# Kernel tuning notes

Measured on AMD Instinct MI355X. Metric: run time of the kernel, lower is better.

The kernel has to match this reference:

```python
import jax, jax.numpy as jnp
import numpy as np

NUM_HEADS = 8
HEAD_DIM = 64      # key_dim = tts_embed_dims // num_heads
TOKEN_NUM = 10
EMBED_DIMS = 512   # tts_embed_dims (num_units)
QUERY_DIM = 256    # tts_embed_dims // 2
BATCH = 131072


def setup_inputs() -> dict:
    key = jax.random.key(0)
    k1, k2, k3, k4 = jax.random.split(key, 4)
    inputs = jax.random.normal(k1, (BATCH, QUERY_DIM), dtype=jnp.float32)
    # nn.Parameter init.normal_(mean=0, std=0.5)
    embed = 0.5 * jax.random.normal(k2, (TOKEN_NUM, HEAD_DIM), dtype=jnp.float32)
    # nn.Linear weights are [out_features, in_features]
    Wq = jax.random.normal(k3, (EMBED_DIMS, QUERY_DIM), dtype=jnp.float32) * (QUERY_DIM ** -0.5)
    Wk = jax.random.normal(k4, (EMBED_DIMS, HEAD_DIM), dtype=jnp.float32) * (HEAD_DIM ** -0.5)
    return {"inputs": inputs, "embed": embed, "Wq": Wq, "Wk": Wk}


def reference(inputs, embed, Wq, Wk):
    # Faithful to this fork: values = raw tanh(embed) keys (W_value unused),
    # and NO softmax on the attention scores.
    N = inputs.shape[0]
    h, d, T = NUM_HEADS, HEAD_DIM, TOKEN_NUM
    keys_raw = jnp.tanh(embed)                       # [T, d] (shared across batch)

    q = inputs @ Wq.T                                # [N, E]
    q = q.reshape(N, h, d)                           # split heads (T_q == 1 squeezed)

    k = keys_raw @ Wk.T                              # [T, E]
    k = k.reshape(T, h, d)                           # [T, h, d]

    scale = HEAD_DIM ** 0.5                          # self.key_dim ** 0.5
    # scores: [h, N, 1, T] -> store as [h, N, T]
    scores = jnp.einsum('nhd,thd->hnt', q, k) / scale

    # out per head: scores @ values, values = keys_raw [T, d]
    out = jnp.einsum('hnt,td->nhd', scores, keys_raw)  # [N, h, d]
    style_embed = out.reshape(N, 1, h * d)             # concat heads -> [N, 1, E]
    attn_score = scores[:, :, None, :]                 # [h, N, 1, T]
    return style_embed, attn_score
```

## Files before the change

kernel.cpp:

```cpp
#include <hip/hip_runtime.h>
#include <math.h>

#define N_QDIM 256
#define N_EDIM 512
#define N_HEADS 8
#define N_HDIM 64
#define N_TOK 10
#define NJ 80

__global__ __launch_bounds__(256) void precompute_kernel(
    const float* __restrict__ embed, const float* __restrict__ Wq,
    const float* __restrict__ Wk, float* __restrict__ Ws,
    float* __restrict__ keysOut)
{
    __shared__ float skeys[N_TOK * N_HDIM];
    __shared__ float sK[N_TOK * N_EDIM];
    const int tid = threadIdx.x;

    for (int i = tid; i < N_TOK * N_HDIM; i += 256) {
        float v = tanhf(embed[i]);
        skeys[i] = v;
        if (blockIdx.x == 0) keysOut[i] = v;
    }
    __syncthreads();

    for (int i = tid; i < N_TOK * N_EDIM; i += 256) {
        int t = i >> 9;
        int e = i & 511;
        float s = 0.f;
        #pragma unroll
        for (int d = 0; d < N_HDIM; d++)
            s += skeys[t * N_HDIM + d] * Wk[e * N_HDIM + d];
        sK[i] = s;
    }
    __syncthreads();

    int v = blockIdx.x * 256 + tid;
    int qd = v / NJ;
    int j  = v - qd * NJ;
    int h  = j / N_TOK;
    int t  = j - h * N_TOK;
    float s = 0.f;
    #pragma unroll
    for (int d = 0; d < N_HDIM; d++)
        s += Wq[(h * N_HDIM + d) * N_QDIM + qd] * sK[t * N_EDIM + h * N_HDIM + d];
    Ws[qd * NJ + j] = s * 0.125f;
}

__global__ __launch_bounds__(256) void main_kernel(
    const float* __restrict__ inputs, const float* __restrict__ Ws,
    const float* __restrict__ keys, float* __restrict__ outStyle,
    float* __restrict__ outAttn, int N)
{
    __shared__ float smem[128 * 81];
    float* sA = smem;
    float* sB = smem + 32 * 132;

    const int tid = threadIdx.x;
    const int tc = tid & 15;
    const int tr = tid >> 4;
    const int n0 = blockIdx.x * 128;
    const float* A = inputs + (size_t)n0 * N_QDIM;

    float acc[8][5];
    #pragma unroll
    for (int i = 0; i < 8; i++)
        #pragma unroll
        for (int j = 0; j < 5; j++) acc[i][j] = 0.f;

    for (int kb = 0; kb < N_QDIM; kb += 32) {
        __syncthreads();
        #pragma unroll
        for (int it = 0; it < 4; it++) {
            int flat = it * 256 + tid;
            int row = flat >> 3;
            int ch  = flat & 7;
            float4 v = *(const float4*)(A + row * N_QDIM + kb + ch * 4);
            int k = ch * 4;
            sA[(k + 0) * 132 + row] = v.x;
            sA[(k + 1) * 132 + row] = v.y;
            sA[(k + 2) * 132 + row] = v.z;
            sA[(k + 3) * 132 + row] = v.w;
        }
        #pragma unroll
        for (int it = 0; it < 3; it++) {
            int f = it * 256 + tid;
            if (f < 640)
                *(float4*)(sB + f * 4) = *(const float4*)(Ws + kb * NJ + f * 4);
        }
        __syncthreads();
        #pragma unroll
        for (int k = 0; k < 32; k++) {
            float4 a0 = *(const float4*)(sA + k * 132 + tr * 8);
            float4 a1 = *(const float4*)(sA + k * 132 + tr * 8 + 4);
            float b[5];
            #pragma unroll
            for (int j = 0; j < 5; j++) b[j] = sB[k * NJ + tc * 5 + j];
            float a[8] = {a0.x, a0.y, a0.z, a0.w, a1.x, a1.y, a1.z, a1.w};
            #pragma unroll
            for (int i = 0; i < 8; i++)
                #pragma unroll
                for (int j = 0; j < 5; j++)
                    acc[i][j] += a[i] * b[j];
        }
    }

    __syncthreads();
    float* sS = smem;
    #pragma unroll
    for (int i = 0; i < 8; i++) {
        int row = tr * 8 + i;
        #pragma unroll
        for (int j = 0; j < 5; j++)
            sS[row * 81 + tc * 5 + j] = acc[i][j];
    }
    __syncthreads();

    #pragma unroll
    for (int h = 0; h < N_HEADS; h++) {
        float* dst = outAttn + (size_t)h * N * N_TOK + (size_t)n0 * N_TOK;
        for (int i = tid; i < 128 * N_TOK; i += 256) {
            int row = i / N_TOK;
            int t = i - row * N_TOK;
            dst[i] = sS[row * 81 + h * N_TOK + t];
        }
    }

    float4 kr[N_TOK];
    #pragma unroll
    for (int t = 0; t < N_TOK; t++)
        kr[t] = *(const float4*)(keys + t * N_HDIM + tc * 4);

    for (int i = 0; i < 8; i++) {
        int row = tr * 8 + i;
        #pragma unroll
        for (int h = 0; h < N_HEADS; h++) {
            float4 o = {0.f, 0.f, 0.f, 0.f};
            #pragma unroll
            for (int t = 0; t < N_TOK; t++) {
                float s = sS[row * 81 + h * N_TOK + t];
                o.x += s * kr[t].x;
                o.y += s * kr[t].y;
                o.z += s * kr[t].z;
                o.w += s * kr[t].w;
            }
            *(float4*)(outStyle + (size_t)(n0 + row) * N_EDIM + h * N_HDIM + tc * 4) = o;
        }
    }
}

extern "C" void kernel_launch(void* const* d_in, const int* in_sizes, int n_in,
                              void* d_out, int out_size, void* d_ws, size_t ws_size,
                              hipStream_t stream) {
    const float* inputs = (const float*)d_in[0];
    const float* embed  = (const float*)d_in[1];
    const float* Wq     = (const float*)d_in[2];
    const float* Wk     = (const float*)d_in[3];

    const int N = in_sizes[0] / N_QDIM;

    float* Ws     = (float*)d_ws;
    float* keysWs = Ws + N_QDIM * NJ;

    float* outStyle = (float*)d_out;
    float* outAttn  = outStyle + (size_t)N * N_EDIM;

    precompute_kernel<<<80, 256, 0, stream>>>(embed, Wq, Wk, Ws, keysWs);
    main_kernel<<<N / 128, 256, 0, stream>>>(inputs, Ws, keysWs, outStyle, outAttn, N);
}
```

Baseline: 521.6 us.

## Use split-bf16 MFMA for the projection GEMM with pre-fragmented weights

Replaces the FP32 register-tiled SIMT GEMM with bf16 MFMA 16x16x32 instructions. Three-term hi/lo bf16 splitting (hi*hi, lo*hi, hi*lo) keeps accuracy close to FP32. The precompute kernel now writes the folded weight matrix already split and laid out in MFMA fragment order, so the main kernel loads A straight from global memory and B as vectors, with no shared-memory staging for the GEMM. The epilogue is restructured per wave, with a smaller shared buffer per wave and a launch-bounds occupancy hint. The cost is extra split arithmetic and a small precision loss.

```diff
diff --git a/kernel.cpp b/kernel.cpp
--- a/kernel.cpp
+++ b/kernel.cpp
@@ -8,10 +8,13 @@
 #define N_TOK 10
 #define NJ 80
 
+typedef short bf16x8 __attribute__((ext_vector_type(8)));
+typedef float f32x4 __attribute__((ext_vector_type(4)));
+
 __global__ __launch_bounds__(256) void precompute_kernel(
     const float* __restrict__ embed, const float* __restrict__ Wq,
-    const float* __restrict__ Wk, float* __restrict__ Ws,
-    float* __restrict__ keysOut)
+    const float* __restrict__ Wk, unsigned short* __restrict__ WfHi,
+    unsigned short* __restrict__ WfLo, float* __restrict__ keysOut)
 {
     __shared__ float skeys[N_TOK * N_HDIM];
     __shared__ float sK[N_TOK * N_EDIM];
@@ -35,117 +38,142 @@
     }
     __syncthreads();
 
-    int v = blockIdx.x * 256 + tid;
-    int qd = v / NJ;
-    int j  = v - qd * NJ;
-    int h  = j / N_TOK;
-    int t  = j - h * N_TOK;
+    int flat = blockIdx.x * 256 + tid;
+    int e    = flat & 7;
+    int lane = (flat >> 3) & 63;
+    int rest = flat >> 9;
+    int n    = rest % 5;
+    int kb   = rest / 5;
+    int c    = n * 16 + (lane & 15);
+    int h    = c / N_TOK;
+    int t    = c - h * N_TOK;
+    int qd   = kb * 32 + (lane >> 4) * 8 + e;
+
     float s = 0.f;
     #pragma unroll
     for (int d = 0; d < N_HDIM; d++)
         s += Wq[(h * N_HDIM + d) * N_QDIM + qd] * sK[t * N_EDIM + h * N_HDIM + d];
-    Ws[qd * NJ + j] = s * 0.125f;
+    s *= 0.125f;
+
+    unsigned int u = __float_as_uint(s);
+    float rem = s - __uint_as_float(u & 0xffff0000u);
+    int idx = ((kb * 5 + n) * 64 + lane) * 8 + e;
+    WfHi[idx] = (unsigned short)(u >> 16);
+    WfLo[idx] = (unsigned short)(__float_as_uint(rem) >> 16);
 }
 
-__global__ __launch_bounds__(256) void main_kernel(
-    const float* __restrict__ inputs, const float* __restrict__ Ws,
-    const float* __restrict__ keys, float* __restrict__ outStyle,
-    float* __restrict__ outAttn, int N)
+static __device__ __forceinline__ void splitFrag(float4 v0, float4 v1,
+                                                 bf16x8& hi, bf16x8& lo)
 {
-    __shared__ float smem[128 * 81];
-    float* sA = smem;
-    float* sB = smem + 32 * 132;
+    float x[8] = {v0.x, v0.y, v0.z, v0.w, v1.x, v1.y, v1.z, v1.w};
+    #pragma unroll
+    for (int e = 0; e < 8; e++) {
+        unsigned u = __float_as_uint(x[e]);
+        hi[e] = (short)(u >> 16);
+        float r = x[e] - __uint_as_float(u & 0xffff0000u);
+        lo[e] = (short)(__float_as_uint(r) >> 16);
+    }
+}
+
+__global__ __launch_bounds__(256, 4) void main_kernel(
+    const float* __restrict__ inputs, const unsigned short* __restrict__ WfHi,
+    const unsigned short* __restrict__ WfLo, const float* __restrict__ keys,
+    float* __restrict__ outStyle, float* __restrict__ outAttn, int N)
+{
+    __shared__ float sS[4][16 * 84];
 
     const int tid = threadIdx.x;
-    const int tc = tid & 15;
-    const int tr = tid >> 4;
-    const int n0 = blockIdx.x * 128;
-    const float* A = inputs + (size_t)n0 * N_QDIM;
+    const int w   = tid >> 6;
+    const int l   = tid & 63;
+    const int l15 = l & 15;
+    const int lg  = l >> 4;
+    const int rowBase = blockIdx.x * 128 + w * 32;
 
-    float acc[8][5];
+    const float* pa0 = inputs + (size_t)(rowBase + l15) * N_QDIM + lg * 8;
+    const float* pa1 = pa0 + 16 * N_QDIM;
+
+    f32x4 acc[2][5];
     #pragma unroll
-    for (int i = 0; i < 8; i++)
+    for (int m = 0; m < 2; m++)
         #pragma unroll
-        for (int j = 0; j < 5; j++) acc[i][j] = 0.f;
+        for (int n = 0; n < 5; n++)
+            acc[m][n] = (f32x4){0.f, 0.f, 0.f, 0.f};
 
-    for (int kb = 0; kb < N_QDIM; kb += 32) {
-        __syncthreads();
+    #pragma unroll 2
+    for (int kb = 0; kb < 8; kb++) {
+        const float* p0 = pa0 + kb * 32;
+        const float* p1 = pa1 + kb * 32;
+        float4 x0 = *(const float4*)(p0);
+        float4 x1 = *(const float4*)(p0 + 4);
+        float4 y0 = *(const float4*)(p1);
+        float4 y1 = *(const float4*)(p1 + 4);
+        bf16x8 a0h, a0l, a1h, a1l;
+        splitFrag(x0, x1, a0h, a0l);
+        splitFrag(y0, y1, a1h, a1l);
+
+        const unsigned short* bh = WfHi + kb * 2560 + l * 8;
+        const unsigned short* bl = WfLo + kb * 2560 + l * 8;
         #pragma unroll
-        for (int it = 0; it < 4; it++) {
-            int flat = it * 256 + tid;
-            int row = flat >> 3;
-            int ch  = flat & 7;
-            float4 v = *(const float4*)(A + row * N_QDIM + kb + ch * 4);
-            int k = ch * 4;
-            sA[(k + 0) * 132 + row] = v.x;
-            sA[(k + 1) * 132 + row] = v.y;
-            sA[(k + 2) * 132 + row] = v.z;
-            sA[(k + 3) * 132 + row] = v.w;
-        }
-        #pragma unroll
-        for (int it = 0; it < 3; it++) {
-            int f = it * 256 + tid;
-            if (f < 640)
-                *(float4*)(sB + f * 4) = *(const float4*)(Ws + kb * NJ + f * 4);
-        }
-        __syncthreads();
-        #pragma unroll
-        for (int k = 0; k < 32; k++) {
-            float4 a0 = *(const float4*)(sA + k * 132 + tr * 8);
-            float4 a1 = *(const float4*)(sA + k * 132 + tr * 8 + 4);
-            float b[5];
-            #pragma unroll
-            for (int j = 0; j < 5; j++) b[j] = sB[k * NJ + tc * 5 + j];
-            float a[8] = {a0.x, a0.y, a0.z, a0.w, a1.x, a1.y, a1.z, a1.w};
-            #pragma unroll
-            for (int i = 0; i < 8; i++)
-                #pragma unroll
-                for (int j = 0; j < 5; j++)
-                    acc[i][j] += a[i] * b[j];
-        }
-    }
-
-    __syncthreads();
-    float* sS = smem;
-    #pragma unroll
-    for (int i = 0; i < 8; i++) {
-        int row = tr * 8 + i;
-        #pragma unroll
-        for (int j = 0; j < 5; j++)
-            sS[row * 81 + tc * 5 + j] = acc[i][j];
-    }
-    __syncthreads();
-
-    #pragma unroll
-    for (int h = 0; h < N_HEADS; h++) {
-        float* dst = outAttn + (size_t)h * N * N_TOK + (size_t)n0 * N_TOK;
-        for (int i = tid; i < 128 * N_TOK; i += 256) {
-            int row = i / N_TOK;
-            int t = i - row * N_TOK;
-            dst[i] = sS[row * 81 + h * N_TOK + t];
+        for (int n = 0; n < 5; n++) {
+            bf16x8 bhi = *(const bf16x8*)(bh + n * 512);
+            bf16x8 blo = *(const bf16x8*)(bl + n * 512);
+            acc[0][n] = __builtin_amdgcn_mfma_f32_16x16x32_bf16(a0h, bhi, acc[0][n], 0, 0, 0);
+            acc[1][n] = __builtin_amdgcn_mfma_f32_16x16x32_bf16(a1h, bhi, acc[1][n], 0, 0, 0);
+            acc[0][n] = __builtin_amdgcn_mfma_f32_16x16x32_bf16(a0l, bhi, acc[0][n], 0, 0, 0);
+            acc[1][n] = __builtin_amdgcn_mfma_f32_16x16x32_bf16(a1l, bhi, acc[1][n], 0, 0, 0);
+            acc[0][n] = __builtin_amdgcn_mfma_f32_16x16x32_bf16(a0h, blo, acc[0][n], 0, 0, 0);
+            acc[1][n] = __builtin_amdgcn_mfma_f32_16x16x32_bf16(a1h, blo, acc[1][n], 0, 0, 0);
         }
     }
 
     float4 kr[N_TOK];
     #pragma unroll
     for (int t = 0; t < N_TOK; t++)
-        kr[t] = *(const float4*)(keys + t * N_HDIM + tc * 4);
+        kr[t] = *(const float4*)(keys + t * N_HDIM + l15 * 4);
 
-    for (int i = 0; i < 8; i++) {
-        int row = tr * 8 + i;
+    float* s = sS[w];
+
+    #pragma unroll
+    for (int m = 0; m < 2; m++) {
+        #pragma unroll
+        for (int n = 0; n < 5; n++)
+            #pragma unroll
+            for (int r = 0; r < 4; r++)
+                s[(lg * 4 + r) * 84 + n * 16 + l15] = acc[m][n][r];
+        __syncthreads();
+
+        const int rStart = rowBase + m * 16;
+
         #pragma unroll
         for (int h = 0; h < N_HEADS; h++) {
-            float4 o = {0.f, 0.f, 0.f, 0.f};
+            float* dst = outAttn + ((size_t)h * N + rStart) * N_TOK;
+            for (int i = l; i < 16 * N_TOK; i += 64) {
+                int rr = i / N_TOK;
+                int t  = i - rr * N_TOK;
+                dst[i] = s[rr * 84 + h * N_TOK + t];
+            }
+        }
+
+        #pragma unroll
+        for (int i = 0; i < 4; i++) {
+            int rr = i * 4 + lg;
+            const float* srow = s + rr * 84;
+            float* orow = outStyle + (size_t)(rStart + rr) * N_EDIM + l15 * 4;
             #pragma unroll
-            for (int t = 0; t < N_TOK; t++) {
-                float s = sS[row * 81 + h * N_TOK + t];
-                o.x += s * kr[t].x;
-                o.y += s * kr[t].y;
-                o.z += s * kr[t].z;
-                o.w += s * kr[t].w;
+            for (int h = 0; h < N_HEADS; h++) {
+                float4 o = {0.f, 0.f, 0.f, 0.f};
+                #pragma unroll
+                for (int t2 = 0; t2 < N_TOK; t2 += 2) {
+                    float2 sc = *(const float2*)(srow + h * N_TOK + t2);
+                    o.x += sc.x * kr[t2].x + sc.y * kr[t2 + 1].x;
+                    o.y += sc.x * kr[t2].y + sc.y * kr[t2 + 1].y;
+                    o.z += sc.x * kr[t2].z + sc.y * kr[t2 + 1].z;
+                    o.w += sc.x * kr[t2].w + sc.y * kr[t2 + 1].w;
+                }
+                *(float4*)(orow + h * N_HDIM) = o;
             }
-            *(float4*)(outStyle + (size_t)(n0 + row) * N_EDIM + h * N_HDIM + tc * 4) = o;
         }
+        __syncthreads();
     }
 }
 
@@ -159,12 +187,13 @@
 
     const int N = in_sizes[0] / N_QDIM;
 
-    float* Ws     = (float*)d_ws;
-    float* keysWs = Ws + N_QDIM * NJ;
+    float* keysWs = (float*)d_ws;
+    unsigned short* WfHi = (unsigned short*)((char*)d_ws + 640 * sizeof(float));
+    unsigned short* WfLo = WfHi + 8 * 5 * 64 * 8;
 
     float* outStyle = (float*)d_out;
     float* outAttn  = outStyle + (size_t)N * N_EDIM;
 
-    precompute_kernel<<<80, 256, 0, stream>>>(embed, Wq, Wk, Ws, keysWs);
-    main_kernel<<<N / 128, 256, 0, stream>>>(inputs, Ws, keysWs, outStyle, outAttn, N);
+    precompute_kernel<<<80, 256, 0, stream>>>(embed, Wq, Wk, WfHi, WfLo, keysWs);
+    main_kernel<<<N / 128, 256, 0, stream>>>(inputs, WfHi, WfLo, keysWs, outStyle, outAttn, N);
 }
```

Result: faster. 457.1 us (-12.4%).
